# Kernel tuning notes

Hardware: AMD Instinct MI355X
Metric: run time of the kernel (lower is better)

## Reference

```python
import jax, jax.numpy as jnp
import numpy as np

N_NODES = 50000
N_EDGES = 800000
F_IN = 256
F_OUT = 256


def setup_inputs() -> dict:
    key = jax.random.key(0)
    k1, k2, k3, k4, k5 = jax.random.split(key, 5)
    x = jax.random.normal(k1, (N_NODES, F_IN), dtype=jnp.float32)
    edge_index = jax.random.randint(k2, (2, N_EDGES), 0, N_NODES, dtype=jnp.int64)
    C_values = jax.random.uniform(k3, (N_EDGES,), dtype=jnp.float32)
    # nn.Linear(input_dim, output_dim) parameters
    W = jax.random.normal(k4, (F_OUT, F_IN), dtype=jnp.float32) / np.sqrt(F_IN)
    b = jax.random.normal(k5, (F_OUT,), dtype=jnp.float32) * 0.01
    return {"x": x, "edge_index": edge_index, "C_values": C_values, "W": W, "b": b}


def reference(x, edge_index, C_values, W, b):
    # gcn_norm(add_self_loops=False): deg = row-sum of edge weights,
    # w_norm[e] = deg[row]^-1/2 * w[e] * deg[col]^-1/2
    row, col = edge_index[0], edge_index[1]
    n = x.shape[0]
    deg = jax.ops.segment_sum(C_values, row, num_segments=n)  # [N]
    deg_inv_sqrt = jnp.where(deg > 0, jax.lax.rsqrt(jnp.where(deg > 0, deg, 1.0)), 0.0)
    w_norm = deg_inv_sqrt[row] * C_values * deg_inv_sqrt[col]  # [E]
    # SpMM: prop_x[i] = sum_{e: row[e]=i} w_norm[e] * x[col[e]]
    prop_x = jax.ops.segment_sum(w_norm[:, None] * x[col], row, num_segments=n)  # [N, F_in]
    # dense linear transform
    return prop_x @ W.T + b  # [N, F_out]
```

## Files before the change

kernel.cpp:

```cpp
#include <hip/hip_runtime.h>
#include <hip/hip_bf16.h>

#define NN 50000
#define NE 800000
#define FD 256
#define NN_PAD 50048
#define SCAN_B 196
#define NPB 16

typedef __attribute__((ext_vector_type(8))) short bf16x8;
typedef __attribute__((ext_vector_type(4))) float f32x4;
typedef unsigned long long ull;

__device__ __forceinline__ short f2bf(float f) {
    union { float f; unsigned u; } v; v.f = f;
    unsigned r = v.u + 0x7fffu + ((v.u >> 16) & 1u);
    return (short)(r >> 16);
}
__device__ __forceinline__ float bf2f(unsigned short u) {
    union { unsigned u; float f; } v; v.u = ((unsigned)u) << 16;
    return v.f;
}

__global__ void count_deg_kernel(const int* __restrict__ row, const float* __restrict__ cv,
                                 ull* __restrict__ dc) {
    int e = blockIdx.x * blockDim.x + threadIdx.x;
    if (e < NE) {
        int r = row[e];
        unsigned cf = (unsigned)(cv[e] * 16777216.0f + 0.5f);
        atomicAdd(&dc[r], (1ULL << 40) | (ull)cf);
    }
}

__device__ __forceinline__ int block_excl_scan256(int v, int tid) {
    __shared__ int ws[4];
    int lane = tid & 63, wv = tid >> 6;
    int incl = v;
#pragma unroll
    for (int off = 1; off < 64; off <<= 1) {
        int t = __shfl_up(incl, off);
        if (lane >= off) incl += t;
    }
    if (lane == 63) ws[wv] = incl;
    __syncthreads();
    int acc = 0;
#pragma unroll
    for (int k = 0; k < 4; ++k) if (k < wv) acc += ws[k];
    return acc + incl - v;
}

__global__ void sum_dinv_kernel(const ull* __restrict__ dc, float* __restrict__ dinv,
                                int* __restrict__ bsum) {
    int i = blockIdx.x * 256 + threadIdx.x;
    ull v = (i < NN) ? dc[i] : 0ULL;
    int cnt = (int)(v >> 40);
    ull df = v & ((1ULL << 40) - 1);
    int lane = threadIdx.x & 63, wv = threadIdx.x >> 6;
    int s = cnt;
#pragma unroll
    for (int off = 1; off < 64; off <<= 1) s += __shfl_xor(s, off);
    __shared__ int ws[4];
    if (lane == 0) ws[wv] = s;
    __syncthreads();
    if (threadIdx.x == 0) bsum[blockIdx.x] = ws[0] + ws[1] + ws[2] + ws[3];
    if (i < NN) {
        float d = (float)df * (1.0f / 16777216.0f);
        dinv[i] = (df > 0) ? rsqrtf(d) : 0.f;
    }
}

__global__ void scan_bsum_kernel(int* __restrict__ bsum) {
    int tid = threadIdx.x;
    int v = (tid < SCAN_B) ? bsum[tid] : 0;
    int excl = block_excl_scan256(v, tid);
    if (tid < SCAN_B) bsum[tid] = excl;
}

__global__ void write_rs_kernel(const ull* __restrict__ dc, const int* __restrict__ bsum,
                                int* __restrict__ rs, int* __restrict__ cursor) {
    int i = blockIdx.x * 256 + threadIdx.x;
    int v = (i < NN) ? (int)(dc[i] >> 40) : 0;
    int excl = block_excl_scan256(v, threadIdx.x) + bsum[blockIdx.x];
    if (i < NN) { rs[i] = excl; cursor[i] = excl; }
    if (i == NN - 1) rs[NN] = excl + v;
}

__global__ void quant_kernel(const float* __restrict__ x, const float* __restrict__ W,
                             const float* __restrict__ dinv, unsigned* __restrict__ q8,
                             float* __restrict__ scale, short* __restrict__ Wb) {
    int wid = blockIdx.x * 4 + (threadIdx.x >> 6);
    int lane = threadIdx.x & 63;
    if (wid < NN) {
        int r = wid;
        float dr = dinv[r];
        float4 v = *(const float4*)(x + (size_t)r * FD + lane * 4);
        v.x *= dr; v.y *= dr; v.z *= dr; v.w *= dr;
        float m = fmaxf(fmaxf(fabsf(v.x), fabsf(v.y)), fmaxf(fabsf(v.z), fabsf(v.w)));
#pragma unroll
        for (int off = 1; off < 64; off <<= 1) m = fmaxf(m, __shfl_xor(m, off, 64));
        float s   = (m > 0.f) ? m * (1.0f / 127.0f) : 1.0f;
        float inv = (m > 0.f) ? 127.0f / m : 0.f;
        if (lane == 0) scale[r] = s;
        int q0 = (int)rintf(v.x * inv) + 128;
        int q1 = (int)rintf(v.y * inv) + 128;
        int q2 = (int)rintf(v.z * inv) + 128;
        int q3 = (int)rintf(v.w * inv) + 128;
        q8[r * 64 + lane] = (unsigned)q0 | ((unsigned)q1 << 8) |
                            ((unsigned)q2 << 16) | ((unsigned)q3 << 24);
    } else {
        int j = (wid - NN) * 64 + lane;
        if (j < FD * FD) Wb[j] = f2bf(W[j]);
    }
}

__global__ void bucket_kernel(const int* __restrict__ row, const int* __restrict__ col,
                              const float* __restrict__ cv, const float* __restrict__ scale,
                              int* __restrict__ cursor, unsigned* __restrict__ e_cw) {
    int e = blockIdx.x * blockDim.x + threadIdx.x;
    if (e >= NE) return;
    int r = row[e], c = col[e];
    float w = cv[e] * scale[c];
    int idx = atomicAdd(&cursor[r], 1);
    unsigned wb = (unsigned)(unsigned short)f2bf(w);
    e_cw[idx] = (wb << 16) | (unsigned)c;
}

__global__ __launch_bounds__(256) void fused_kernel(
        const unsigned* __restrict__ q8, const unsigned* __restrict__ e_cw,
        const int* __restrict__ rs, const float* __restrict__ dinv,
        const short* __restrict__ Wb, const float* __restrict__ bias,
        float* __restrict__ out) {
    __shared__ short Ab[NPB][264];
    int tid = threadIdx.x, lane = tid & 63, wv = tid >> 6;
    int q = lane >> 4, i = lane & 15;
    int nbase = blockIdx.x * NPB;
    int n = nbase + wv * 4 + q;

    int e = rs[n], en = rs[n + 1];
    const unsigned* xq = q8 + i * 4;

    float acc[16];
#pragma unroll
    for (int k = 0; k < 16; ++k) acc[k] = 0.f;
    float wsum = 0.f;

#define EDGE(V, CW) do {                                                     \
        float w_ = bf2f((unsigned short)((CW) >> 16));                       \
        wsum += w_;                                                          \
        acc[0]  = fmaf(w_, (float)(unsigned char)((V).x      ), acc[0]);     \
        acc[1]  = fmaf(w_, (float)(unsigned char)((V).x >>  8), acc[1]);     \
        acc[2]  = fmaf(w_, (float)(unsigned char)((V).x >> 16), acc[2]);     \
        acc[3]  = fmaf(w_, (float)((V).x >> 24), acc[3]);                    \
        acc[4]  = fmaf(w_, (float)(unsigned char)((V).y      ), acc[4]);     \
        acc[5]  = fmaf(w_, (float)(unsigned char)((V).y >>  8), acc[5]);     \
        acc[6]  = fmaf(w_, (float)(unsigned char)((V).y >> 16), acc[6]);     \
        acc[7]  = fmaf(w_, (float)((V).y >> 24), acc[7]);                    \
        acc[8]  = fmaf(w_, (float)(unsigned char)((V).z      ), acc[8]);     \
        acc[9]  = fmaf(w_, (float)(unsigned char)((V).z >>  8), acc[9]);     \
        acc[10] = fmaf(w_, (float)(unsigned char)((V).z >> 16), acc[10]);    \
        acc[11] = fmaf(w_, (float)((V).z >> 24), acc[11]);                   \
        acc[12] = fmaf(w_, (float)(unsigned char)((V).w      ), acc[12]);    \
        acc[13] = fmaf(w_, (float)(unsigned char)((V).w >>  8), acc[13]);    \
        acc[14] = fmaf(w_, (float)(unsigned char)((V).w >> 16), acc[14]);    \
        acc[15] = fmaf(w_, (float)((V).w >> 24), acc[15]);                   \
    } while (0)

    while (e < en && (e & 3)) {
        unsigned cw = e_cw[e];
        uint4 v = *(const uint4*)(xq + (size_t)(cw & 0xFFFFu) * 64);
        EDGE(v, cw);
        ++e;
    }
    for (; e + 4 <= en; e += 4) {
        uint4 cw4 = *(const uint4*)(e_cw + e);
        uint4 v0 = *(const uint4*)(xq + (size_t)(cw4.x & 0xFFFFu) * 64);
        uint4 v1 = *(const uint4*)(xq + (size_t)(cw4.y & 0xFFFFu) * 64);
        uint4 v2 = *(const uint4*)(xq + (size_t)(cw4.z & 0xFFFFu) * 64);
        uint4 v3 = *(const uint4*)(xq + (size_t)(cw4.w & 0xFFFFu) * 64);
        EDGE(v0, cw4.x);
        EDGE(v1, cw4.y);
        EDGE(v2, cw4.z);
        EDGE(v3, cw4.w);
    }
    for (; e < en; ++e) {
        unsigned cw = e_cw[e];
        uint4 v = *(const uint4*)(xq + (size_t)(cw & 0xFFFFu) * 64);
        EDGE(v, cw);
    }
#undef EDGE

    {
        float dr = dinv[n];
        float base = 128.f * wsum;
        bf16x8 lo, hi;
#pragma unroll
        for (int k = 0; k < 8; ++k) {
            lo[k] = f2bf((acc[k] - base) * dr);
            hi[k] = f2bf((acc[k + 8] - base) * dr);
        }
        *(bf16x8*)&Ab[wv * 4 + q][i * 16] = lo;
        *(bf16x8*)&Ab[wv * 4 + q][i * 16 + 8] = hi;
    }
    __syncthreads();

    int m = lane & 15, g = lane >> 4;
    f32x4 acc0 = {0,0,0,0}, acc1 = {0,0,0,0}, acc2 = {0,0,0,0}, acc3 = {0,0,0,0};
    const short* w0 = Wb + (size_t)(wv * 64 + 0  + m) * FD;
    const short* w1 = Wb + (size_t)(wv * 64 + 16 + m) * FD;
    const short* w2 = Wb + (size_t)(wv * 64 + 32 + m) * FD;
    const short* w3 = Wb + (size_t)(wv * 64 + 48 + m) * FD;
#pragma unroll
    for (int ks = 0; ks < 8; ++ks) {
        int ko = ks * 32 + g * 8;
        bf16x8 af = *(const bf16x8*)&Ab[m][ko];
        bf16x8 b0 = *(const bf16x8*)(w0 + ko);
        bf16x8 b1 = *(const bf16x8*)(w1 + ko);
        bf16x8 b2 = *(const bf16x8*)(w2 + ko);
        bf16x8 b3 = *(const bf16x8*)(w3 + ko);
        acc0 = __builtin_amdgcn_mfma_f32_16x16x32_bf16(af, b0, acc0, 0, 0, 0);
        acc1 = __builtin_amdgcn_mfma_f32_16x16x32_bf16(af, b1, acc1, 0, 0, 0);
        acc2 = __builtin_amdgcn_mfma_f32_16x16x32_bf16(af, b2, acc2, 0, 0, 0);
        acc3 = __builtin_amdgcn_mfma_f32_16x16x32_bf16(af, b3, acc3, 0, 0, 0);
    }
#pragma unroll
    for (int nt = 0; nt < 4; ++nt) {
        f32x4 a = nt == 0 ? acc0 : nt == 1 ? acc1 : nt == 2 ? acc2 : acc3;
        int c = wv * 64 + nt * 16 + m;
        float bv = bias[c];
#pragma unroll
        for (int r = 0; r < 4; ++r) {
            out[(size_t)(nbase + g * 4 + r) * FD + c] = a[r] + bv;
        }
    }
}

extern "C" void kernel_launch(void* const* d_in, const int* in_sizes, int n_in,
                              void* d_out, int out_size, void* d_ws, size_t ws_size,
                              hipStream_t stream) {
    const float* x  = (const float*)d_in[0];
    const int*   ei = (const int*)d_in[1];
    const float* cv = (const float*)d_in[2];
    const float* W  = (const float*)d_in[3];
    const float* b  = (const float*)d_in[4];
    float* out = (float*)d_out;

    const int* row = ei;
    const int* col = ei + NE;

    ull*      dc     = (ull*)d_ws;
    unsigned* e_cw   = (unsigned*)(dc + NN_PAD);
    unsigned* q8     = e_cw + NE;
    short*    Wb     = (short*)(q8 + (size_t)NN * 64);
    float*    dinv   = (float*)(Wb + (size_t)FD * FD);
    float*    scale  = dinv + NN_PAD;
    int*      rs     = (int*)(scale + NN_PAD);
    int*      cursor = rs + NN_PAD;
    int*      bsum   = cursor + NN_PAD;

    hipMemsetAsync(dc, 0, NN_PAD * sizeof(ull), stream);

    count_deg_kernel<<<(NE + 255) / 256, 256, 0, stream>>>(row, cv, dc);
    sum_dinv_kernel<<<SCAN_B, 256, 0, stream>>>(dc, dinv, bsum);
    scan_bsum_kernel<<<1, 256, 0, stream>>>(bsum);
    write_rs_kernel<<<SCAN_B, 256, 0, stream>>>(dc, bsum, rs, cursor);
    quant_kernel<<<NN / 4 + 256, 256, 0, stream>>>(x, W, dinv, q8, scale, Wb);
    bucket_kernel<<<(NE + 255) / 256, 256, 0, stream>>>(row, col, cv, scale, cursor, e_cw);

    fused_kernel<<<NN / NPB, 256, 0, stream>>>(q8, e_cw, rs, dinv, Wb, b, out);
}
```

Measured before the change: 187.0 us.

## Process each node with a full wavefront split across edges; fold bsum scan into write_rs

The gather now has all four 16-lane groups of a wavefront share one node's edge list, each group taking every fourth edge, with partial sums combined by cross-lane shuffles. Previously each group handled its own node. Walking the four nodes in turn balances work when degrees differ and issues more independent row loads. Separately, the one-block scan of block sums is merged into write_rs_kernel, where every block redundantly rescans the 196 sums, saving one kernel launch. The costs are the shuffle reductions per node and the serial walk over four nodes per wavefront.

Measured after the change: 192.6 us. 3.0% more time.

```diff
diff --git a/kernel.cpp b/kernel.cpp
--- a/kernel.cpp
+++ b/kernel.cpp
@@ -69,18 +69,17 @@
     }
 }
 
-__global__ void scan_bsum_kernel(int* __restrict__ bsum) {
-    int tid = threadIdx.x;
-    int v = (tid < SCAN_B) ? bsum[tid] : 0;
-    int excl = block_excl_scan256(v, tid);
-    if (tid < SCAN_B) bsum[tid] = excl;
-}
-
 __global__ void write_rs_kernel(const ull* __restrict__ dc, const int* __restrict__ bsum,
                                 int* __restrict__ rs, int* __restrict__ cursor) {
-    int i = blockIdx.x * 256 + threadIdx.x;
+    __shared__ int sb[SCAN_B];
+    int tid = threadIdx.x;
+    int bv = (tid < SCAN_B) ? bsum[tid] : 0;
+    int excl_b = block_excl_scan256(bv, tid);
+    if (tid < SCAN_B) sb[tid] = excl_b;
+    __syncthreads();
+    int i = blockIdx.x * 256 + tid;
     int v = (i < NN) ? (int)(dc[i] >> 40) : 0;
-    int excl = block_excl_scan256(v, threadIdx.x) + bsum[blockIdx.x];
+    int excl = block_excl_scan256(v, tid) + sb[blockIdx.x];
     if (i < NN) { rs[i] = excl; cursor[i] = excl; }
     if (i == NN - 1) rs[NN] = excl + v;
 }
@@ -132,17 +131,9 @@
         float* __restrict__ out) {
     __shared__ short Ab[NPB][264];
     int tid = threadIdx.x, lane = tid & 63, wv = tid >> 6;
-    int q = lane >> 4, i = lane & 15;
+    int g = lane >> 4, i = lane & 15;
     int nbase = blockIdx.x * NPB;
-    int n = nbase + wv * 4 + q;
-
-    int e = rs[n], en = rs[n + 1];
     const unsigned* xq = q8 + i * 4;
-
-    float acc[16];
-#pragma unroll
-    for (int k = 0; k < 16; ++k) acc[k] = 0.f;
-    float wsum = 0.f;
 
 #define EDGE(V, CW) do {                                                     \
         float w_ = bf2f((unsigned short)((CW) >> 16));                       \
@@ -165,45 +156,67 @@
         acc[15] = fmaf(w_, (float)((V).w >> 24), acc[15]);                   \
     } while (0)
 
-    while (e < en && (e & 3)) {
-        unsigned cw = e_cw[e];
-        uint4 v = *(const uint4*)(xq + (size_t)(cw & 0xFFFFu) * 64);
-        EDGE(v, cw);
-        ++e;
-    }
-    for (; e + 4 <= en; e += 4) {
-        uint4 cw4 = *(const uint4*)(e_cw + e);
-        uint4 v0 = *(const uint4*)(xq + (size_t)(cw4.x & 0xFFFFu) * 64);
-        uint4 v1 = *(const uint4*)(xq + (size_t)(cw4.y & 0xFFFFu) * 64);
-        uint4 v2 = *(const uint4*)(xq + (size_t)(cw4.z & 0xFFFFu) * 64);
-        uint4 v3 = *(const uint4*)(xq + (size_t)(cw4.w & 0xFFFFu) * 64);
-        EDGE(v0, cw4.x);
-        EDGE(v1, cw4.y);
-        EDGE(v2, cw4.z);
-        EDGE(v3, cw4.w);
-    }
-    for (; e < en; ++e) {
-        unsigned cw = e_cw[e];
-        uint4 v = *(const uint4*)(xq + (size_t)(cw & 0xFFFFu) * 64);
-        EDGE(v, cw);
+#pragma unroll
+    for (int j = 0; j < 4; ++j) {
+        int n = nbase + wv * 4 + j;
+        int e = rs[n], en = rs[n + 1];
+
+        float acc[16];
+#pragma unroll
+        for (int k = 0; k < 16; ++k) acc[k] = 0.f;
+        float wsum = 0.f;
+
+        for (; e + 16 <= en; e += 16) {
+            unsigned cw0 = e_cw[e + g];
+            unsigned cw1 = e_cw[e + 4 + g];
+            unsigned cw2 = e_cw[e + 8 + g];
+            unsigned cw3 = e_cw[e + 12 + g];
+            uint4 v0 = *(const uint4*)(xq + (size_t)(cw0 & 0xFFFFu) * 64);
+            uint4 v1 = *(const uint4*)(xq + (size_t)(cw1 & 0xFFFFu) * 64);
+            uint4 v2 = *(const uint4*)(xq + (size_t)(cw2 & 0xFFFFu) * 64);
+            uint4 v3 = *(const uint4*)(xq + (size_t)(cw3 & 0xFFFFu) * 64);
+            EDGE(v0, cw0);
+            EDGE(v1, cw1);
+            EDGE(v2, cw2);
+            EDGE(v3, cw3);
+        }
+        for (; e + 4 <= en; e += 4) {
+            unsigned cw = e_cw[e + g];
+            uint4 v = *(const uint4*)(xq + (size_t)(cw & 0xFFFFu) * 64);
+            EDGE(v, cw);
+        }
+        int rem = en - e;
+        if (g < rem) {
+            unsigned cw = e_cw[e + g];
+            uint4 v = *(const uint4*)(xq + (size_t)(cw & 0xFFFFu) * 64);
+            EDGE(v, cw);
+        }
+
+#pragma unroll
+        for (int k = 0; k < 16; ++k) {
+            acc[k] += __shfl_xor(acc[k], 16);
+            acc[k] += __shfl_xor(acc[k], 32);
+        }
+        wsum += __shfl_xor(wsum, 16);
+        wsum += __shfl_xor(wsum, 32);
+
+        if (g == 0) {
+            float dr = dinv[n];
+            float base = 128.f * wsum;
+            bf16x8 lo, hi;
+#pragma unroll
+            for (int k = 0; k < 8; ++k) {
+                lo[k] = f2bf((acc[k] - base) * dr);
+                hi[k] = f2bf((acc[k + 8] - base) * dr);
+            }
+            *(bf16x8*)&Ab[wv * 4 + j][i * 16] = lo;
+            *(bf16x8*)&Ab[wv * 4 + j][i * 16 + 8] = hi;
+        }
     }
 #undef EDGE
-
-    {
-        float dr = dinv[n];
-        float base = 128.f * wsum;
-        bf16x8 lo, hi;
-#pragma unroll
-        for (int k = 0; k < 8; ++k) {
-            lo[k] = f2bf((acc[k] - base) * dr);
-            hi[k] = f2bf((acc[k + 8] - base) * dr);
-        }
-        *(bf16x8*)&Ab[wv * 4 + q][i * 16] = lo;
-        *(bf16x8*)&Ab[wv * 4 + q][i * 16 + 8] = hi;
-    }
-    __syncthreads();
-
-    int m = lane & 15, g = lane >> 4;
+    __syncthreads();
+
+    int m = lane & 15, gg = lane >> 4;
     f32x4 acc0 = {0,0,0,0}, acc1 = {0,0,0,0}, acc2 = {0,0,0,0}, acc3 = {0,0,0,0};
     const short* w0 = Wb + (size_t)(wv * 64 + 0  + m) * FD;
     const short* w1 = Wb + (size_t)(wv * 64 + 16 + m) * FD;
@@ -211,7 +224,7 @@
     const short* w3 = Wb + (size_t)(wv * 64 + 48 + m) * FD;
 #pragma unroll
     for (int ks = 0; ks < 8; ++ks) {
-        int ko = ks * 32 + g * 8;
+        int ko = ks * 32 + gg * 8;
         bf16x8 af = *(const bf16x8*)&Ab[m][ko];
         bf16x8 b0 = *(const bf16x8*)(w0 + ko);
         bf16x8 b1 = *(const bf16x8*)(w1 + ko);
@@ -229,7 +242,7 @@
         float bv = bias[c];
 #pragma unroll
         for (int r = 0; r < 4; ++r) {
-            out[(size_t)(nbase + g * 4 + r) * FD + c] = a[r] + bv;
+            out[(size_t)(nbase + gg * 4 + r) * FD + c] = a[r] + bv;
         }
     }
 }
@@ -261,7 +274,6 @@
 
     count_deg_kernel<<<(NE + 255) / 256, 256, 0, stream>>>(row, cv, dc);
     sum_dinv_kernel<<<SCAN_B, 256, 0, stream>>>(dc, dinv, bsum);
-    scan_bsum_kernel<<<1, 256, 0, stream>>>(bsum);
     write_rs_kernel<<<SCAN_B, 256, 0, stream>>>(dc, bsum, rs, cursor);
     quant_kernel<<<NN / 4 + 256, 256, 0, stream>>>(x, W, dinv, q8, scale, Wb);
     bucket_kernel<<<(NE + 255) / 256, 256, 0, stream>>>(row, col, cv, scale, cursor, e_cw);
```

## Double nodes per block to 32 with 512 threads and fold bsum scan into write_rs

Applied to the files above, without the earlier changes.

The fused SpMM+GEMM kernel now handles 32 nodes per block with 8 waves, split into 2 row groups by 4 column groups. Each W tile loaded from global memory is therefore reused across twice as many rows, which halves the per-node W traffic. Padding nodes are handled with rs entries set to NE, a guarded dinv read and guarded output writes. The separate single-block bsum scan launch is removed: every write_rs block now redundantly scans the 196 block sums itself, saving one launch at the cost of a little duplicated work.

Result: slower. 195.8 us (+4.7%).

```diff
diff --git a/kernel.cpp b/kernel.cpp
--- a/kernel.cpp
+++ b/kernel.cpp
@@ -6,7 +6,7 @@
 #define FD 256
 #define NN_PAD 50048
 #define SCAN_B 196
-#define NPB 16
+#define NPB 32
 
 typedef __attribute__((ext_vector_type(8))) short bf16x8;
 typedef __attribute__((ext_vector_type(4))) float f32x4;
@@ -69,20 +69,20 @@
     }
 }
 
-__global__ void scan_bsum_kernel(int* __restrict__ bsum) {
-    int tid = threadIdx.x;
-    int v = (tid < SCAN_B) ? bsum[tid] : 0;
-    int excl = block_excl_scan256(v, tid);
-    if (tid < SCAN_B) bsum[tid] = excl;
-}
-
 __global__ void write_rs_kernel(const ull* __restrict__ dc, const int* __restrict__ bsum,
                                 int* __restrict__ rs, int* __restrict__ cursor) {
-    int i = blockIdx.x * 256 + threadIdx.x;
+    __shared__ int sb[SCAN_B];
+    int tid = threadIdx.x;
+    int bv = (tid < SCAN_B) ? bsum[tid] : 0;
+    int excl_b = block_excl_scan256(bv, tid);
+    if (tid < SCAN_B) sb[tid] = excl_b;
+    __syncthreads();
+    int i = blockIdx.x * 256 + tid;
     int v = (i < NN) ? (int)(dc[i] >> 40) : 0;
-    int excl = block_excl_scan256(v, threadIdx.x) + bsum[blockIdx.x];
+    int excl = block_excl_scan256(v, tid) + sb[blockIdx.x];
     if (i < NN) { rs[i] = excl; cursor[i] = excl; }
     if (i == NN - 1) rs[NN] = excl + v;
+    if (i > NN && i <= NN_PAD) rs[i] = NE;
 }
 
 __global__ void quant_kernel(const float* __restrict__ x, const float* __restrict__ W,
@@ -125,7 +125,7 @@
     e_cw[idx] = (wb << 16) | (unsigned)c;
 }
 
-__global__ __launch_bounds__(256) void fused_kernel(
+__global__ __launch_bounds__(512) void fused_kernel(
         const unsigned* __restrict__ q8, const unsigned* __restrict__ e_cw,
         const int* __restrict__ rs, const float* __restrict__ dinv,
         const short* __restrict__ Wb, const float* __restrict__ bias,
@@ -190,7 +190,7 @@
 #undef EDGE
 
     {
-        float dr = dinv[n];
+        float dr = (n < NN) ? dinv[n] : 0.f;
         float base = 128.f * wsum;
         bf16x8 lo, hi;
 #pragma unroll
@@ -203,16 +203,17 @@
     }
     __syncthreads();
 
+    int wr = wv >> 2, wc = wv & 3;
     int m = lane & 15, g = lane >> 4;
     f32x4 acc0 = {0,0,0,0}, acc1 = {0,0,0,0}, acc2 = {0,0,0,0}, acc3 = {0,0,0,0};
-    const short* w0 = Wb + (size_t)(wv * 64 + 0  + m) * FD;
-    const short* w1 = Wb + (size_t)(wv * 64 + 16 + m) * FD;
-    const short* w2 = Wb + (size_t)(wv * 64 + 32 + m) * FD;
-    const short* w3 = Wb + (size_t)(wv * 64 + 48 + m) * FD;
+    const short* w0 = Wb + (size_t)(wc * 64 + 0  + m) * FD;
+    const short* w1 = Wb + (size_t)(wc * 64 + 16 + m) * FD;
+    const short* w2 = Wb + (size_t)(wc * 64 + 32 + m) * FD;
+    const short* w3 = Wb + (size_t)(wc * 64 + 48 + m) * FD;
 #pragma unroll
     for (int ks = 0; ks < 8; ++ks) {
         int ko = ks * 32 + g * 8;
-        bf16x8 af = *(const bf16x8*)&Ab[m][ko];
+        bf16x8 af = *(const bf16x8*)&Ab[wr * 16 + m][ko];
         bf16x8 b0 = *(const bf16x8*)(w0 + ko);
         bf16x8 b1 = *(const bf16x8*)(w1 + ko);
         bf16x8 b2 = *(const bf16x8*)(w2 + ko);
@@ -225,11 +226,12 @@
 #pragma unroll
     for (int nt = 0; nt < 4; ++nt) {
         f32x4 a = nt == 0 ? acc0 : nt == 1 ? acc1 : nt == 2 ? acc2 : acc3;
-        int c = wv * 64 + nt * 16 + m;
+        int c = wc * 64 + nt * 16 + m;
         float bv = bias[c];
 #pragma unroll
         for (int r = 0; r < 4; ++r) {
-            out[(size_t)(nbase + g * 4 + r) * FD + c] = a[r] + bv;
+            int orow = nbase + wr * 16 + g * 4 + r;
+            if (orow < NN) out[(size_t)orow * FD + c] = a[r] + bv;
         }
     }
 }
@@ -254,17 +256,16 @@
     float*    dinv   = (float*)(Wb + (size_t)FD * FD);
     float*    scale  = dinv + NN_PAD;
     int*      rs     = (int*)(scale + NN_PAD);
-    int*      cursor = rs + NN_PAD;
+    int*      cursor = rs + NN_PAD + 64;
     int*      bsum   = cursor + NN_PAD;
 
     hipMemsetAsync(dc, 0, NN_PAD * sizeof(ull), stream);
 
     count_deg_kernel<<<(NE + 255) / 256, 256, 0, stream>>>(row, cv, dc);
     sum_dinv_kernel<<<SCAN_B, 256, 0, stream>>>(dc, dinv, bsum);
-    scan_bsum_kernel<<<1, 256, 0, stream>>>(bsum);
     write_rs_kernel<<<SCAN_B, 256, 0, stream>>>(dc, bsum, rs, cursor);
     quant_kernel<<<NN / 4 + 256, 256, 0, stream>>>(x, W, dinv, q8, scale, Wb);
     bucket_kernel<<<(NE + 255) / 256, 256, 0, stream>>>(row, col, cv, scale, cursor, e_cw);
 
-    fused_kernel<<<NN / NPB, 256, 0, stream>>>(q8, e_cw, rs, dinv, Wb, b, out);
-}
+    fused_kernel<<<(NN + NPB - 1) / NPB, 512, 0, stream>>>(q8, e_cw, rs, dinv, Wb, b, out);
+}
```

## Merge preprocessing kernels into one cooperative kernel with grid syncs

Applied to the files above, without the earlier changes.

Replaces the memset and six preprocessing kernel launches (degree count, dinv/block sums, scan, row-start write, quantization, bucketing) with a single cooperative kernel of 512 blocks that separates phases with grid.sync(). The goal is to remove per-launch overhead and inter-kernel gaps, and it also overlaps the row-start write with quantization. It adds a launch-bounds occupancy hint on the fused SpMM kernel. In exchange, the grid-stride loops run on fewer blocks, which may reduce parallelism for the atomic-heavy edge phases, and each grid barrier has its own cost.

Measured after the change: 442.9 us. 2.37x slower.

```diff
diff --git a/kernel.cpp b/kernel.cpp
--- a/kernel.cpp
+++ b/kernel.cpp
@@ -1,5 +1,8 @@
 #include <hip/hip_runtime.h>
 #include <hip/hip_bf16.h>
+#include <hip/hip_cooperative_groups.h>
+
+namespace cg = cooperative_groups;
 
 #define NN 50000
 #define NE 800000
@@ -7,6 +10,7 @@
 #define NN_PAD 50048
 #define SCAN_B 196
 #define NPB 16
+#define BGRID 512
 
 typedef __attribute__((ext_vector_type(8))) short bf16x8;
 typedef __attribute__((ext_vector_type(4))) float f32x4;
@@ -22,16 +26,6 @@
     return v.f;
 }
 
-__global__ void count_deg_kernel(const int* __restrict__ row, const float* __restrict__ cv,
-                                 ull* __restrict__ dc) {
-    int e = blockIdx.x * blockDim.x + threadIdx.x;
-    if (e < NE) {
-        int r = row[e];
-        unsigned cf = (unsigned)(cv[e] * 16777216.0f + 0.5f);
-        atomicAdd(&dc[r], (1ULL << 40) | (ull)cf);
-    }
-}
-
 __device__ __forceinline__ int block_excl_scan256(int v, int tid) {
     __shared__ int ws[4];
     int lane = tid & 63, wv = tid >> 6;
@@ -49,83 +43,98 @@
     return acc + incl - v;
 }
 
-__global__ void sum_dinv_kernel(const ull* __restrict__ dc, float* __restrict__ dinv,
-                                int* __restrict__ bsum) {
-    int i = blockIdx.x * 256 + threadIdx.x;
-    ull v = (i < NN) ? dc[i] : 0ULL;
-    int cnt = (int)(v >> 40);
-    ull df = v & ((1ULL << 40) - 1);
-    int lane = threadIdx.x & 63, wv = threadIdx.x >> 6;
-    int s = cnt;
-#pragma unroll
-    for (int off = 1; off < 64; off <<= 1) s += __shfl_xor(s, off);
-    __shared__ int ws[4];
-    if (lane == 0) ws[wv] = s;
-    __syncthreads();
-    if (threadIdx.x == 0) bsum[blockIdx.x] = ws[0] + ws[1] + ws[2] + ws[3];
-    if (i < NN) {
-        float d = (float)df * (1.0f / 16777216.0f);
-        dinv[i] = (df > 0) ? rsqrtf(d) : 0.f;
-    }
-}
-
-__global__ void scan_bsum_kernel(int* __restrict__ bsum) {
-    int tid = threadIdx.x;
-    int v = (tid < SCAN_B) ? bsum[tid] : 0;
-    int excl = block_excl_scan256(v, tid);
-    if (tid < SCAN_B) bsum[tid] = excl;
-}
-
-__global__ void write_rs_kernel(const ull* __restrict__ dc, const int* __restrict__ bsum,
-                                int* __restrict__ rs, int* __restrict__ cursor) {
-    int i = blockIdx.x * 256 + threadIdx.x;
-    int v = (i < NN) ? (int)(dc[i] >> 40) : 0;
-    int excl = block_excl_scan256(v, threadIdx.x) + bsum[blockIdx.x];
-    if (i < NN) { rs[i] = excl; cursor[i] = excl; }
-    if (i == NN - 1) rs[NN] = excl + v;
-}
-
-__global__ void quant_kernel(const float* __restrict__ x, const float* __restrict__ W,
-                             const float* __restrict__ dinv, unsigned* __restrict__ q8,
-                             float* __restrict__ scale, short* __restrict__ Wb) {
-    int wid = blockIdx.x * 4 + (threadIdx.x >> 6);
-    int lane = threadIdx.x & 63;
-    if (wid < NN) {
-        int r = wid;
-        float dr = dinv[r];
-        float4 v = *(const float4*)(x + (size_t)r * FD + lane * 4);
-        v.x *= dr; v.y *= dr; v.z *= dr; v.w *= dr;
-        float m = fmaxf(fmaxf(fabsf(v.x), fabsf(v.y)), fmaxf(fabsf(v.z), fabsf(v.w)));
-#pragma unroll
-        for (int off = 1; off < 64; off <<= 1) m = fmaxf(m, __shfl_xor(m, off, 64));
-        float s   = (m > 0.f) ? m * (1.0f / 127.0f) : 1.0f;
-        float inv = (m > 0.f) ? 127.0f / m : 0.f;
-        if (lane == 0) scale[r] = s;
-        int q0 = (int)rintf(v.x * inv) + 128;
-        int q1 = (int)rintf(v.y * inv) + 128;
-        int q2 = (int)rintf(v.z * inv) + 128;
-        int q3 = (int)rintf(v.w * inv) + 128;
-        q8[r * 64 + lane] = (unsigned)q0 | ((unsigned)q1 << 8) |
-                            ((unsigned)q2 << 16) | ((unsigned)q3 << 24);
-    } else {
-        int j = (wid - NN) * 64 + lane;
-        if (j < FD * FD) Wb[j] = f2bf(W[j]);
-    }
-}
-
-__global__ void bucket_kernel(const int* __restrict__ row, const int* __restrict__ col,
-                              const float* __restrict__ cv, const float* __restrict__ scale,
-                              int* __restrict__ cursor, unsigned* __restrict__ e_cw) {
-    int e = blockIdx.x * blockDim.x + threadIdx.x;
-    if (e >= NE) return;
-    int r = row[e], c = col[e];
-    float w = cv[e] * scale[c];
-    int idx = atomicAdd(&cursor[r], 1);
-    unsigned wb = (unsigned)(unsigned short)f2bf(w);
-    e_cw[idx] = (wb << 16) | (unsigned)c;
-}
-
-__global__ __launch_bounds__(256) void fused_kernel(
+__global__ void build_kernel(const int* __restrict__ row, const int* __restrict__ col,
+                             const float* __restrict__ cv, const float* __restrict__ x,
+                             const float* __restrict__ W,
+                             ull* __restrict__ dc, float* __restrict__ dinv,
+                             float* __restrict__ scale, int* __restrict__ rs,
+                             int* __restrict__ cursor, int* __restrict__ bsum,
+                             unsigned* __restrict__ q8, short* __restrict__ Wb,
+                             unsigned* __restrict__ e_cw) {
+    cg::grid_group grid = cg::this_grid();
+    const int gsz = gridDim.x * blockDim.x;
+    const int gtid = blockIdx.x * blockDim.x + threadIdx.x;
+    const int tid = threadIdx.x;
+
+    for (int i = gtid; i < NN_PAD; i += gsz) dc[i] = 0ULL;
+    for (int j = gtid; j < FD * FD; j += gsz) Wb[j] = f2bf(W[j]);
+    grid.sync();
+
+    for (int e = gtid; e < NE; e += gsz) {
+        int r = row[e];
+        unsigned cf = (unsigned)(cv[e] * 16777216.0f + 0.5f);
+        atomicAdd(&dc[r], (1ULL << 40) | (ull)cf);
+    }
+    grid.sync();
+
+    if (blockIdx.x < SCAN_B) {
+        int i = blockIdx.x * 256 + tid;
+        ull v = (i < NN) ? dc[i] : 0ULL;
+        int cnt = (int)(v >> 40);
+        ull df = v & ((1ULL << 40) - 1);
+        int lane = tid & 63, wv = tid >> 6;
+        int s = cnt;
+#pragma unroll
+        for (int off = 1; off < 64; off <<= 1) s += __shfl_xor(s, off);
+        __shared__ int ws2[4];
+        if (lane == 0) ws2[wv] = s;
+        __syncthreads();
+        if (tid == 0) bsum[blockIdx.x] = ws2[0] + ws2[1] + ws2[2] + ws2[3];
+        if (i < NN) {
+            float d = (float)df * (1.0f / 16777216.0f);
+            dinv[i] = (df > 0) ? rsqrtf(d) : 0.f;
+        }
+    }
+    grid.sync();
+
+    if (blockIdx.x == 0) {
+        int v = (tid < SCAN_B) ? bsum[tid] : 0;
+        int excl = block_excl_scan256(v, tid);
+        if (tid < SCAN_B) bsum[tid] = excl;
+    }
+    grid.sync();
+
+    if (blockIdx.x < SCAN_B) {
+        int i = blockIdx.x * 256 + tid;
+        int v = (i < NN) ? (int)(dc[i] >> 40) : 0;
+        int excl = block_excl_scan256(v, tid) + bsum[blockIdx.x];
+        if (i < NN) { rs[i] = excl; cursor[i] = excl; }
+        if (i == NN - 1) rs[NN] = excl + v;
+        if (i > NN && i <= NN_PAD) rs[i] = NE;
+    }
+    {
+        int gw = gtid >> 6, nw = gsz >> 6;
+        int lane = tid & 63;
+        for (int r = gw; r < NN; r += nw) {
+            float dr = dinv[r];
+            float4 v = *(const float4*)(x + (size_t)r * FD + lane * 4);
+            v.x *= dr; v.y *= dr; v.z *= dr; v.w *= dr;
+            float m = fmaxf(fmaxf(fabsf(v.x), fabsf(v.y)), fmaxf(fabsf(v.z), fabsf(v.w)));
+#pragma unroll
+            for (int off = 1; off < 64; off <<= 1) m = fmaxf(m, __shfl_xor(m, off, 64));
+            float s   = (m > 0.f) ? m * (1.0f / 127.0f) : 1.0f;
+            float inv = (m > 0.f) ? 127.0f / m : 0.f;
+            if (lane == 0) scale[r] = s;
+            int q0 = (int)rintf(v.x * inv) + 128;
+            int q1 = (int)rintf(v.y * inv) + 128;
+            int q2 = (int)rintf(v.z * inv) + 128;
+            int q3 = (int)rintf(v.w * inv) + 128;
+            q8[r * 64 + lane] = (unsigned)q0 | ((unsigned)q1 << 8) |
+                                ((unsigned)q2 << 16) | ((unsigned)q3 << 24);
+        }
+    }
+    grid.sync();
+
+    for (int e = gtid; e < NE; e += gsz) {
+        int r = row[e], c = col[e];
+        float w = cv[e] * scale[c];
+        int idx = atomicAdd(&cursor[r], 1);
+        unsigned wb = (unsigned)(unsigned short)f2bf(w);
+        e_cw[idx] = (wb << 16) | (unsigned)c;
+    }
+}
+
+__global__ __launch_bounds__(256, 6) void fused_kernel(
         const unsigned* __restrict__ q8, const unsigned* __restrict__ e_cw,
         const int* __restrict__ rs, const float* __restrict__ dinv,
         const short* __restrict__ Wb, const float* __restrict__ bias,
@@ -254,17 +263,16 @@
     float*    dinv   = (float*)(Wb + (size_t)FD * FD);
     float*    scale  = dinv + NN_PAD;
     int*      rs     = (int*)(scale + NN_PAD);
-    int*      cursor = rs + NN_PAD;
+    int*      cursor = rs + NN_PAD + 64;
     int*      bsum   = cursor + NN_PAD;
 
-    hipMemsetAsync(dc, 0, NN_PAD * sizeof(ull), stream);
-
-    count_deg_kernel<<<(NE + 255) / 256, 256, 0, stream>>>(row, cv, dc);
-    sum_dinv_kernel<<<SCAN_B, 256, 0, stream>>>(dc, dinv, bsum);
-    scan_bsum_kernel<<<1, 256, 0, stream>>>(bsum);
-    write_rs_kernel<<<SCAN_B, 256, 0, stream>>>(dc, bsum, rs, cursor);
-    quant_kernel<<<NN / 4 + 256, 256, 0, stream>>>(x, W, dinv, q8, scale, Wb);
-    bucket_kernel<<<(NE + 255) / 256, 256, 0, stream>>>(row, col, cv, scale, cursor, e_cw);
+    void* args[] = {
+        (void*)&row, (void*)&col, (void*)&cv, (void*)&x, (void*)&W,
+        (void*)&dc, (void*)&dinv, (void*)&scale, (void*)&rs,
+        (void*)&cursor, (void*)&bsum, (void*)&q8, (void*)&Wb, (void*)&e_cw
+    };
+    hipLaunchCooperativeKernel((const void*)build_kernel, dim3(BGRID), dim3(256),
+                               args, 0, stream);
 
     fused_kernel<<<NN / NPB, 256, 0, stream>>>(q8, e_cw, rs, dinv, Wb, b, out);
 }
```
